# Kernel optimization log

Measured on AMD Instinct MI355X. Metric: run time of the kernel, lower is better.

## Reference

```python
import jax, jax.numpy as jnp
import numpy as np

N, D, C = 4096, 512, 100
EPS = 1e-8


def setup_inputs() -> dict:
    key = jax.random.key(0)
    k1, k2 = jax.random.split(key)
    X = jax.random.normal(k1, (N, D), dtype=jnp.float32)
    # torch.rand -> uniform [0, 1), shape (1, hiddensize, classes)
    grp = jax.random.uniform(k2, (1, D, C), dtype=jnp.float32)
    return {"X": X, "grp": grp}


def reference(X, grp):
    # L1 distance of each sample to each class prototype: [N, D, 1] - [1, D, C] -> sum over D -> [N, C]
    l1 = jnp.abs(X[:, :, None] - grp).sum(axis=1)
    norm = jax.nn.softmax(-l1, axis=1)  # Softmin over classes

    # Cosine similarity between X [N, D] and prototypes grp[0] [D, C] -> [N, C]
    g = grp[0]
    dot = X @ g  # [N, C]
    xn = jnp.sqrt(jnp.sum(X * X, axis=1, keepdims=True))      # [N, 1]
    gn = jnp.sqrt(jnp.sum(g * g, axis=0, keepdims=True))      # [1, C]
    cs = dot / jnp.maximum(xn * gn, EPS)

    confidence = jnp.max(cs, axis=1, keepdims=True)  # [N, 1]
    confusion = jax.nn.softmax(cs, axis=1)           # [N, C]
    return confidence * confusion * norm
```

## Files before the change

kernel.cpp:

```cpp
#include <hip/hip_runtime.h>

typedef float v2f __attribute__((ext_vector_type(2)));

#define D_DIM 512
#define C_CLS 100
#define SAMP 4
#define NT 256

__global__ __launch_bounds__(NT, 4) void cls_kernel(const float* __restrict__ X,
                                                    const float* __restrict__ grp,
                                                    float* __restrict__ out) {
    __shared__ float xs[SAMP][520];
    __shared__ float part[8][25][36];
    __shared__ float redA[SAMP][25];
    __shared__ float redB[SAMP][25];
    __shared__ float xsqs[SAMP];

    const int t = threadIdx.x;
    const int n0 = blockIdx.x * SAMP;

    {
        const float4* Xv = (const float4*)(X + (size_t)n0 * D_DIM);
#pragma unroll
        for (int i = t; i < SAMP * D_DIM / 4; i += NT) {
            int row = i >> 7;
            int col = i & 127;
            *(float4*)&xs[row][col * 4] = Xv[i];
        }
    }
    __syncthreads();

    if (t < 128) {
        const int r = t >> 5, j = t & 31;
        float v = 0.f;
#pragma unroll
        for (int k = 0; k < 4; ++k) {
            float4 a = *(const float4*)&xs[r][j * 4 + k * 128];
            v += a.x * a.x + a.y * a.y + a.z * a.z + a.w * a.w;
        }
#pragma unroll
        for (int m = 16; m > 0; m >>= 1) v += __shfl_xor(v, m, 32);
        if (j == 0) xsqs[r] = v;
    }

    const bool act = (t < 200);
    const int dq = t / 25;
    const int cq = t - dq * 25;

    float l1[4][4];
    v2f dtl[4], dth[4];
    v2f gsql = {0.f, 0.f}, gsqh = {0.f, 0.f};
#pragma unroll
    for (int i = 0; i < 4; ++i) {
        dtl[i] = (v2f){0.f, 0.f};
        dth[i] = (v2f){0.f, 0.f};
#pragma unroll
        for (int j = 0; j < 4; ++j) l1[i][j] = 0.f;
    }

    if (act) {
        const float* gp = grp + cq * 4;
        const int dbase = dq * 64;
#pragma unroll 2
        for (int dd = 0; dd < 64; dd += 4) {
            const int d4 = dbase + dd;
            float xr[4][4];
#pragma unroll
            for (int si = 0; si < 4; ++si)
                *(float4*)&xr[si][0] = *(const float4*)&xs[si][d4];
#pragma unroll
            for (int k = 0; k < 4; ++k) {
                float4 g = *(const float4*)&gp[(d4 + k) * C_CLS];
                v2f glo = {g.x, g.y};
                v2f ghi = {g.z, g.w};
                gsql += glo * glo;
                gsqh += ghi * ghi;
#pragma unroll
                for (int si = 0; si < 4; ++si) {
                    float x = xr[si][k];
                    v2f x2 = {x, x};
                    v2f el = x2 - glo;
                    v2f eh = x2 - ghi;
                    l1[si][0] += fabsf(el.x);
                    l1[si][1] += fabsf(el.y);
                    l1[si][2] += fabsf(eh.x);
                    l1[si][3] += fabsf(eh.y);
                    dtl[si] += x2 * glo;
                    dth[si] += x2 * ghi;
                }
            }
        }
        float* p = &part[dq][cq][0];
#pragma unroll
        for (int si = 0; si < 4; ++si) {
            *(float4*)&p[si * 4]      = float4{l1[si][0], l1[si][1], l1[si][2], l1[si][3]};
            *(float4*)&p[16 + si * 4] = float4{dtl[si].x, dtl[si].y, dth[si].x, dth[si].y};
        }
        *(float4*)&p[32] = float4{gsql.x, gsql.y, gsqh.x, gsqh.y};
    }
    __syncthreads();

    const int s  = t / 25;
    const int c2 = t - s * 25;
    const bool act2 = (t < 100);

    float l1c[4] = {0.f, 0.f, 0.f, 0.f};
    float dtc[4] = {0.f, 0.f, 0.f, 0.f};
    float gsc[4] = {0.f, 0.f, 0.f, 0.f};
    if (act2) {
#pragma unroll
        for (int q = 0; q < 8; ++q) {
            const float* p = &part[q][c2][0];
            float4 a = *(const float4*)&p[s * 4];
            float4 b = *(const float4*)&p[16 + s * 4];
            float4 c = *(const float4*)&p[32];
            l1c[0] += a.x; l1c[1] += a.y; l1c[2] += a.z; l1c[3] += a.w;
            dtc[0] += b.x; dtc[1] += b.y; dtc[2] += b.z; dtc[3] += b.w;
            gsc[0] += c.x; gsc[1] += c.y; gsc[2] += c.z; gsc[3] += c.w;
        }
    }

    float cs[4] = {0.f, 0.f, 0.f, 0.f};
    if (act2) {
        float xq = xsqs[s];
#pragma unroll
        for (int c = 0; c < 4; ++c)
            cs[c] = dtc[c] / fmaxf(sqrtf(xq * gsc[c]), 1e-8f);
        redA[s][c2] = fminf(fminf(l1c[0], l1c[1]), fminf(l1c[2], l1c[3]));
        redB[s][c2] = fmaxf(fmaxf(cs[0], cs[1]), fmaxf(cs[2], cs[3]));
    }
    __syncthreads();

    float minl1 = 0.f, maxcs = 0.f;
    if (act2) {
        minl1 = redA[s][0];
        maxcs = redB[s][0];
        for (int k = 1; k < 25; ++k) {
            minl1 = fminf(minl1, redA[s][k]);
            maxcs = fmaxf(maxcs, redB[s][k]);
        }
    }
    __syncthreads();

    if (act2) {
        redA[s][c2] = __expf(minl1 - l1c[0]) + __expf(minl1 - l1c[1]) +
                      __expf(minl1 - l1c[2]) + __expf(minl1 - l1c[3]);
        redB[s][c2] = __expf(cs[0] - maxcs) + __expf(cs[1] - maxcs) +
                      __expf(cs[2] - maxcs) + __expf(cs[3] - maxcs);
    }
    __syncthreads();

    if (act2) {
        float s1 = 0.f, s2 = 0.f;
        for (int k = 0; k < 25; ++k) { s1 += redA[s][k]; s2 += redB[s][k]; }
        float f = maxcs / (s1 * s2);
        float4 o;
        o.x = f * __expf(cs[0] - maxcs) * __expf(minl1 - l1c[0]);
        o.y = f * __expf(cs[1] - maxcs) * __expf(minl1 - l1c[1]);
        o.z = f * __expf(cs[2] - maxcs) * __expf(minl1 - l1c[2]);
        o.w = f * __expf(cs[3] - maxcs) * __expf(minl1 - l1c[3]);
        *(float4*)&out[(size_t)(n0 + s) * C_CLS + c2 * 4] = o;
    }
}

extern "C" void kernel_launch(void* const* d_in, const int* in_sizes, int n_in,
                              void* d_out, int out_size, void* d_ws, size_t ws_size,
                              hipStream_t stream) {
    const float* X   = (const float*)d_in[0];
    const float* grp = (const float*)d_in[1];
    float* out = (float*)d_out;
    (void)d_ws; (void)ws_size;

    cls_kernel<<<4096 / SAMP, NT, 0, stream>>>(X, grp, out);
}
```

Measured before the change: 32.90 us.

## Stage prototype chunks into LDS with async double buffering and eight samples per block

Each block now handles 8 samples instead of 4. The prototype matrix is streamed in 64-row chunks into a double-buffered LDS area with global_load_lds, so the next chunk loads while the current one is computed. X is read directly from global memory rather than staged in LDS. Each wave covers a quarter of each chunk for all 8 samples, which halves the grid, and the partial-sum buffers reuse the staging memory through a union. The cost is a waitcnt plus barrier per chunk, lanes 50-63 of each wave idle, and fewer blocks to fill the GPU.

```diff
diff --git a/kernel.cpp b/kernel.cpp
--- a/kernel.cpp
+++ b/kernel.cpp
@@ -4,48 +4,64 @@
 
 #define D_DIM 512
 #define C_CLS 100
-#define SAMP 4
+#define SAMP 8
 #define NT 256
+#define BD 64
+#define NCHUNK (D_DIM / BD)
+
+struct SMem {
+    union {
+        float4 g[2][BD * 25];
+        struct {
+            float4 A[SAMP][4][25];
+            float4 B[SAMP][4][25];
+            float4 G[4][25];
+        } p;
+    } u;
+    float redA[SAMP][25];
+    float redB[SAMP][25];
+    float xsqs[SAMP];
+};
+
+__device__ static inline void load16_lds(const float* g, void* l) {
+    __builtin_amdgcn_global_load_lds(
+        (const __attribute__((address_space(1))) unsigned int*)g,
+        (__attribute__((address_space(3))) unsigned int*)l, 16, 0, 0);
+}
+
+#define STAGE(buf, c)                                                          \
+    for (int iss = wv; iss < 25; iss += 4)                                     \
+        load16_lds(grp + (size_t)(c) * (BD * C_CLS) + iss * 256 + lane * 4,    \
+                   (void*)&sm.u.g[buf][iss * 64]);
 
 __global__ __launch_bounds__(NT, 4) void cls_kernel(const float* __restrict__ X,
                                                     const float* __restrict__ grp,
                                                     float* __restrict__ out) {
-    __shared__ float xs[SAMP][520];
-    __shared__ float part[8][25][36];
-    __shared__ float redA[SAMP][25];
-    __shared__ float redB[SAMP][25];
-    __shared__ float xsqs[SAMP];
+    __shared__ SMem sm;
 
     const int t = threadIdx.x;
+    const int lane = t & 63;
+    const int wv = t >> 6;
     const int n0 = blockIdx.x * SAMP;
 
+    STAGE(0, 0)
+
     {
-        const float4* Xv = (const float4*)(X + (size_t)n0 * D_DIM);
-#pragma unroll
-        for (int i = t; i < SAMP * D_DIM / 4; i += NT) {
-            int row = i >> 7;
-            int col = i & 127;
-            *(float4*)&xs[row][col * 4] = Xv[i];
-        }
-    }
-    __syncthreads();
-
-    if (t < 128) {
         const int r = t >> 5, j = t & 31;
         float v = 0.f;
 #pragma unroll
         for (int k = 0; k < 4; ++k) {
-            float4 a = *(const float4*)&xs[r][j * 4 + k * 128];
+            float4 a = *(const float4*)&X[(size_t)(n0 + r) * D_DIM + j * 4 + k * 128];
             v += a.x * a.x + a.y * a.y + a.z * a.z + a.w * a.w;
         }
 #pragma unroll
         for (int m = 16; m > 0; m >>= 1) v += __shfl_xor(v, m, 32);
-        if (j == 0) xsqs[r] = v;
-    }
-
-    const bool act = (t < 200);
-    const int dq = t / 25;
-    const int cq = t - dq * 25;
+        if (j == 0) sm.xsqs[r] = v;
+    }
+
+    const int cq = lane % 25;
+    const int sg = lane / 25;
+    const bool cact = (lane < 50);
 
     float l1[4][4];
     v2f dtl[4], dth[4];
@@ -58,62 +74,80 @@
         for (int j = 0; j < 4; ++j) l1[i][j] = 0.f;
     }
 
-    if (act) {
-        const float* gp = grp + cq * 4;
-        const int dbase = dq * 64;
+    asm volatile("s_waitcnt vmcnt(0)" ::: "memory");
+    __syncthreads();
+
+    const float* xb = X + (size_t)(n0 + sg * 4) * D_DIM;
+
+    int cb = 0;
+#pragma unroll 1
+    for (int c = 0; c < NCHUNK; ++c) {
+        if (c + 1 < NCHUNK) { STAGE(cb ^ 1, c + 1) }
+
+        if (cact) {
+            const float4* gbase = &sm.u.g[cb][wv * 16 * 25 + cq];
+            const int dglob = c * BD + wv * 16;
 #pragma unroll 2
-        for (int dd = 0; dd < 64; dd += 4) {
-            const int d4 = dbase + dd;
-            float xr[4][4];
-#pragma unroll
-            for (int si = 0; si < 4; ++si)
-                *(float4*)&xr[si][0] = *(const float4*)&xs[si][d4];
-#pragma unroll
-            for (int k = 0; k < 4; ++k) {
-                float4 g = *(const float4*)&gp[(d4 + k) * C_CLS];
-                v2f glo = {g.x, g.y};
-                v2f ghi = {g.z, g.w};
-                gsql += glo * glo;
-                gsqh += ghi * ghi;
-#pragma unroll
-                for (int si = 0; si < 4; ++si) {
-                    float x = xr[si][k];
-                    v2f x2 = {x, x};
-                    v2f el = x2 - glo;
-                    v2f eh = x2 - ghi;
-                    l1[si][0] += fabsf(el.x);
-                    l1[si][1] += fabsf(el.y);
-                    l1[si][2] += fabsf(eh.x);
-                    l1[si][3] += fabsf(eh.y);
-                    dtl[si] += x2 * glo;
-                    dth[si] += x2 * ghi;
+            for (int dd4 = 0; dd4 < 16; dd4 += 4) {
+                float xr[4][4];
+#pragma unroll
+                for (int si = 0; si < 4; ++si)
+                    *(float4*)&xr[si][0] =
+                        *(const float4*)&xb[si * D_DIM + dglob + dd4];
+#pragma unroll
+                for (int k = 0; k < 4; ++k) {
+                    float4 g4 = gbase[(dd4 + k) * 25];
+                    v2f glo = {g4.x, g4.y};
+                    v2f ghi = {g4.z, g4.w};
+                    gsql += glo * glo;
+                    gsqh += ghi * ghi;
+#pragma unroll
+                    for (int si = 0; si < 4; ++si) {
+                        float x = xr[si][k];
+                        v2f x2 = {x, x};
+                        v2f el = x2 - glo;
+                        v2f eh = x2 - ghi;
+                        l1[si][0] += fabsf(el.x);
+                        l1[si][1] += fabsf(el.y);
+                        l1[si][2] += fabsf(eh.x);
+                        l1[si][3] += fabsf(eh.y);
+                        dtl[si] += x2 * glo;
+                        dth[si] += x2 * ghi;
+                    }
                 }
             }
         }
-        float* p = &part[dq][cq][0];
+        asm volatile("s_waitcnt vmcnt(0)" ::: "memory");
+        __syncthreads();
+        cb ^= 1;
+    }
+
+    if (cact) {
 #pragma unroll
         for (int si = 0; si < 4; ++si) {
-            *(float4*)&p[si * 4]      = float4{l1[si][0], l1[si][1], l1[si][2], l1[si][3]};
-            *(float4*)&p[16 + si * 4] = float4{dtl[si].x, dtl[si].y, dth[si].x, dth[si].y};
-        }
-        *(float4*)&p[32] = float4{gsql.x, gsql.y, gsqh.x, gsqh.y};
+            sm.u.p.A[sg * 4 + si][wv][cq] =
+                float4{l1[si][0], l1[si][1], l1[si][2], l1[si][3]};
+            sm.u.p.B[sg * 4 + si][wv][cq] =
+                float4{dtl[si].x, dtl[si].y, dth[si].x, dth[si].y};
+        }
+        if (sg == 0)
+            sm.u.p.G[wv][cq] = float4{gsql.x, gsql.y, gsqh.x, gsqh.y};
     }
     __syncthreads();
 
     const int s  = t / 25;
     const int c2 = t - s * 25;
-    const bool act2 = (t < 100);
+    const bool act2 = (t < 200);
 
     float l1c[4] = {0.f, 0.f, 0.f, 0.f};
     float dtc[4] = {0.f, 0.f, 0.f, 0.f};
     float gsc[4] = {0.f, 0.f, 0.f, 0.f};
     if (act2) {
 #pragma unroll
-        for (int q = 0; q < 8; ++q) {
-            const float* p = &part[q][c2][0];
-            float4 a = *(const float4*)&p[s * 4];
-            float4 b = *(const float4*)&p[16 + s * 4];
-            float4 c = *(const float4*)&p[32];
+        for (int q = 0; q < 4; ++q) {
+            float4 a = sm.u.p.A[s][q][c2];
+            float4 b = sm.u.p.B[s][q][c2];
+            float4 c = sm.u.p.G[q][c2];
             l1c[0] += a.x; l1c[1] += a.y; l1c[2] += a.z; l1c[3] += a.w;
             dtc[0] += b.x; dtc[1] += b.y; dtc[2] += b.z; dtc[3] += b.w;
             gsc[0] += c.x; gsc[1] += c.y; gsc[2] += c.z; gsc[3] += c.w;
@@ -122,37 +156,37 @@
 
     float cs[4] = {0.f, 0.f, 0.f, 0.f};
     if (act2) {
-        float xq = xsqs[s];
+        float xq = sm.xsqs[s];
 #pragma unroll
         for (int c = 0; c < 4; ++c)
             cs[c] = dtc[c] / fmaxf(sqrtf(xq * gsc[c]), 1e-8f);
-        redA[s][c2] = fminf(fminf(l1c[0], l1c[1]), fminf(l1c[2], l1c[3]));
-        redB[s][c2] = fmaxf(fmaxf(cs[0], cs[1]), fmaxf(cs[2], cs[3]));
+        sm.redA[s][c2] = fminf(fminf(l1c[0], l1c[1]), fminf(l1c[2], l1c[3]));
+        sm.redB[s][c2] = fmaxf(fmaxf(cs[0], cs[1]), fmaxf(cs[2], cs[3]));
     }
     __syncthreads();
 
     float minl1 = 0.f, maxcs = 0.f;
     if (act2) {
-        minl1 = redA[s][0];
-        maxcs = redB[s][0];
+        minl1 = sm.redA[s][0];
+        maxcs = sm.redB[s][0];
         for (int k = 1; k < 25; ++k) {
-            minl1 = fminf(minl1, redA[s][k]);
-            maxcs = fmaxf(maxcs, redB[s][k]);
-        }
-    }
-    __syncthreads();
-
-    if (act2) {
-        redA[s][c2] = __expf(minl1 - l1c[0]) + __expf(minl1 - l1c[1]) +
-                      __expf(minl1 - l1c[2]) + __expf(minl1 - l1c[3]);
-        redB[s][c2] = __expf(cs[0] - maxcs) + __expf(cs[1] - maxcs) +
-                      __expf(cs[2] - maxcs) + __expf(cs[3] - maxcs);
+            minl1 = fminf(minl1, sm.redA[s][k]);
+            maxcs = fmaxf(maxcs, sm.redB[s][k]);
+        }
+    }
+    __syncthreads();
+
+    if (act2) {
+        sm.redA[s][c2] = __expf(minl1 - l1c[0]) + __expf(minl1 - l1c[1]) +
+                         __expf(minl1 - l1c[2]) + __expf(minl1 - l1c[3]);
+        sm.redB[s][c2] = __expf(cs[0] - maxcs) + __expf(cs[1] - maxcs) +
+                         __expf(cs[2] - maxcs) + __expf(cs[3] - maxcs);
     }
     __syncthreads();
 
     if (act2) {
         float s1 = 0.f, s2 = 0.f;
-        for (int k = 0; k < 25; ++k) { s1 += redA[s][k]; s2 += redB[s][k]; }
+        for (int k = 0; k < 25; ++k) { s1 += sm.redA[s][k]; s2 += sm.redB[s][k]; }
         float f = maxcs / (s1 * s2);
         float4 o;
         o.x = f * __expf(cs[0] - maxcs) * __expf(minl1 - l1c[0]);
```

Result: slower. 38.21 us (+16.2%).

## Read X directly from global memory and interleave the D split across thread groups

Applied to the files above, without the earlier changes.

Drops the shared-memory staging of the four X rows and the barrier after it, so threads load X straight from global (through the caches) inside the main loop. The D-dimension split is interleaved (stride 32 across the eight groups) rather than split into contiguous 64-wide chunks. The partial-sum buffers become separate float4 arrays laid out for the reduction reads, and the launch-bounds occupancy hint rises from 4 to 6. It trades the LDS footprint and a sync for redundant global or L1 reads of X across the 25 class groups, plus possible register pressure from the higher occupancy target.

```diff
diff --git a/kernel.cpp b/kernel.cpp
--- a/kernel.cpp
+++ b/kernel.cpp
@@ -7,35 +7,26 @@
 #define SAMP 4
 #define NT 256
 
-__global__ __launch_bounds__(NT, 4) void cls_kernel(const float* __restrict__ X,
+__global__ __launch_bounds__(NT, 6) void cls_kernel(const float* __restrict__ X,
                                                     const float* __restrict__ grp,
                                                     float* __restrict__ out) {
-    __shared__ float xs[SAMP][520];
-    __shared__ float part[8][25][36];
+    __shared__ float4 pA[SAMP][8][25];
+    __shared__ float4 pB[SAMP][8][25];
+    __shared__ float4 pG[8][25];
     __shared__ float redA[SAMP][25];
     __shared__ float redB[SAMP][25];
     __shared__ float xsqs[SAMP];
 
     const int t = threadIdx.x;
     const int n0 = blockIdx.x * SAMP;
-
-    {
-        const float4* Xv = (const float4*)(X + (size_t)n0 * D_DIM);
-#pragma unroll
-        for (int i = t; i < SAMP * D_DIM / 4; i += NT) {
-            int row = i >> 7;
-            int col = i & 127;
-            *(float4*)&xs[row][col * 4] = Xv[i];
-        }
-    }
-    __syncthreads();
+    const float* xb = X + (size_t)n0 * D_DIM;
 
     if (t < 128) {
         const int r = t >> 5, j = t & 31;
         float v = 0.f;
 #pragma unroll
         for (int k = 0; k < 4; ++k) {
-            float4 a = *(const float4*)&xs[r][j * 4 + k * 128];
+            float4 a = *(const float4*)&xb[(size_t)r * D_DIM + j * 4 + k * 128];
             v += a.x * a.x + a.y * a.y + a.z * a.z + a.w * a.w;
         }
 #pragma unroll
@@ -60,19 +51,18 @@
 
     if (act) {
         const float* gp = grp + cq * 4;
-        const int dbase = dq * 64;
 #pragma unroll 2
-        for (int dd = 0; dd < 64; dd += 4) {
-            const int d4 = dbase + dd;
+        for (int j = 0; j < 16; ++j) {
+            const int d4 = j * 32 + dq * 4;
             float xr[4][4];
 #pragma unroll
             for (int si = 0; si < 4; ++si)
-                *(float4*)&xr[si][0] = *(const float4*)&xs[si][d4];
+                *(float4*)&xr[si][0] = *(const float4*)&xb[si * D_DIM + d4];
 #pragma unroll
             for (int k = 0; k < 4; ++k) {
-                float4 g = *(const float4*)&gp[(d4 + k) * C_CLS];
-                v2f glo = {g.x, g.y};
-                v2f ghi = {g.z, g.w};
+                float4 g4 = *(const float4*)&gp[(d4 + k) * C_CLS];
+                v2f glo = {g4.x, g4.y};
+                v2f ghi = {g4.z, g4.w};
                 gsql += glo * glo;
                 gsqh += ghi * ghi;
 #pragma unroll
@@ -90,13 +80,12 @@
                 }
             }
         }
-        float* p = &part[dq][cq][0];
 #pragma unroll
         for (int si = 0; si < 4; ++si) {
-            *(float4*)&p[si * 4]      = float4{l1[si][0], l1[si][1], l1[si][2], l1[si][3]};
-            *(float4*)&p[16 + si * 4] = float4{dtl[si].x, dtl[si].y, dth[si].x, dth[si].y};
+            pA[si][dq][cq] = float4{l1[si][0], l1[si][1], l1[si][2], l1[si][3]};
+            pB[si][dq][cq] = float4{dtl[si].x, dtl[si].y, dth[si].x, dth[si].y};
         }
-        *(float4*)&p[32] = float4{gsql.x, gsql.y, gsqh.x, gsqh.y};
+        pG[dq][cq] = float4{gsql.x, gsql.y, gsqh.x, gsqh.y};
     }
     __syncthreads();
 
@@ -110,10 +99,9 @@
     if (act2) {
 #pragma unroll
         for (int q = 0; q < 8; ++q) {
-            const float* p = &part[q][c2][0];
-            float4 a = *(const float4*)&p[s * 4];
-            float4 b = *(const float4*)&p[16 + s * 4];
-            float4 c = *(const float4*)&p[32];
+            float4 a = pA[s][q][c2];
+            float4 b = pB[s][q][c2];
+            float4 c = pG[q][c2];
             l1c[0] += a.x; l1c[1] += a.y; l1c[2] += a.z; l1c[3] += a.w;
             dtc[0] += b.x; dtc[1] += b.y; dtc[2] += b.z; dtc[3] += b.w;
             gsc[0] += c.x; gsc[1] += c.y; gsc[2] += c.z; gsc[3] += c.w;
```

New measurement: 35.77 us. 8.7% more time.
